# Kernel tuning notes

Hardware: AMD Instinct MI355X
Metric: run time of the kernel (lower is better)

Reference implementation:

```python
import jax, jax.numpy as jnp
import numpy as np

N_NODES = 100000
N_EDGES = 3200000
N_FEAT = 128
HIDDEN = 16
N_CLASSES = 10
N_GRAPHS = 64


def gcn_conv(x, W, b, src, dst, num_nodes):
    # PyG GCNConv: h = x W; add self-loops; norm = deg^{-1/2}[src]*deg^{-1/2}[dst]
    h = x @ W  # [N, out]
    deg = jax.ops.segment_sum(jnp.ones(src.shape[0], h.dtype), dst,
                              num_segments=num_nodes) + 1.0  # self-loop
    dinv = jax.lax.rsqrt(deg)
    coef = dinv[src] * dinv[dst]  # [E]
    agg = jax.ops.segment_sum(h[src] * coef[:, None], dst,
                              num_segments=num_nodes)
    # self-loop contribution: norm = dinv[i]^2
    agg = agg + h * (dinv * dinv)[:, None]
    return agg + b


def setup_inputs() -> dict:
    key = jax.random.key(0)
    k1, k2, k3, k4, k5, k6, k7 = jax.random.split(key, 7)
    x = jax.random.normal(k1, (N_NODES, N_FEAT), dtype=jnp.float32)
    edge_index = jax.random.randint(k2, (2, N_EDGES), 0, N_NODES, dtype=jnp.int64)
    batch = jnp.sort(jax.random.randint(k3, (N_NODES,), 0, N_GRAPHS, dtype=jnp.int64))
    W1 = jax.random.normal(k4, (N_FEAT, HIDDEN), dtype=jnp.float32) / np.sqrt(N_FEAT)
    b1 = jnp.zeros((HIDDEN,), jnp.float32)
    W2 = jax.random.normal(k5, (HIDDEN, N_CLASSES), dtype=jnp.float32) / np.sqrt(HIDDEN)
    b2 = jnp.zeros((N_CLASSES,), jnp.float32)
    return {"x": x, "edge_index": edge_index, "batch": batch,
            "W1": W1, "b1": b1, "W2": W2, "b2": b2}


def reference(x, edge_index, batch, W1, b1, W2, b2):
    src, dst = edge_index[0], edge_index[1]
    h = gcn_conv(x, W1, b1, src, dst, N_NODES)
    h = jax.nn.relu(h)
    h = gcn_conv(h, W2, b2, src, dst, N_NODES)  # [N, C]
    # global mean pool per graph
    sums = jax.ops.segment_sum(h, batch, num_segments=N_GRAPHS)
    cnts = jax.ops.segment_sum(jnp.ones(N_NODES, h.dtype), batch,
                               num_segments=N_GRAPHS)
    pooled = sums / jnp.maximum(cnts, 1.0)[:, None]  # [G, C]
    return jax.nn.log_softmax(pooled, axis=1)
```

## Files before the change

kernel.cpp:

```cpp
#include <hip/hip_runtime.h>

#define N_NODES   100000
#define N_EDGES   3200000
#define N_FEAT    128
#define HIDDEN    16
#define N_CLASSES 10
#define N_GRAPHS  64

#define NBUCK     391
#define CAP       9216
#define BINA_EPB  8192
#define BINA_BLOCKS ((N_EDGES + BINA_EPB - 1) / BINA_EPB)


__global__ __launch_bounds__(512) void k_ginit(int* __restrict__ gcur,
                                               float* __restrict__ pooled) {
    int t = threadIdx.x;
    if (t < NBUCK) gcur[t] = t * CAP;
    pooled[t] = 0.f;
    pooled[t + 512] = 0.f;
}

__global__ __launch_bounds__(512) void k_binA(const int* __restrict__ src,
                                              const int* __restrict__ dst,
                                              int* __restrict__ gcur,
                                              int* __restrict__ stage) {
    __shared__ int hist[NBUCK];
    __shared__ int curb[NBUCK];
    int tid = threadIdx.x;
    long long base = (long long)blockIdx.x * BINA_EPB;
    for (int t = tid; t < NBUCK; t += 512) hist[t] = 0;
    __syncthreads();
    int se[16], de[16];
#pragma unroll
    for (int i = 0; i < 16; ++i) {
        long long e = base + i * 512 + tid;
        if (e < N_EDGES) {
            se[i] = src[e];
            de[i] = dst[e];
            atomicAdd(&hist[de[i] >> 8], 1);
        } else {
            de[i] = -1;
        }
    }
    __syncthreads();
    for (int t = tid; t < NBUCK; t += 512) {
        int h = hist[t];
        curb[t] = h ? atomicAdd(&gcur[t], h) : 0;
    }
    __syncthreads();
#pragma unroll
    for (int i = 0; i < 16; ++i) {
        if (de[i] >= 0) {
            int b = de[i] >> 8;
            int p = atomicAdd(&curb[b], 1);
            stage[p] = (se[i] << 8) | (de[i] & 255);
        }
    }
}

__global__ __launch_bounds__(512) void k_bscan(const int* __restrict__ gcur,
                                               int* __restrict__ bbase,
                                               int* __restrict__ off) {
    __shared__ int s[512];
    int t = threadIdx.x;
    int c = (t < NBUCK) ? (gcur[t] - t * CAP) : 0;
    s[t] = c;
    __syncthreads();
    for (int o = 1; o < 512; o <<= 1) {
        int a = (t >= o) ? s[t - o] : 0;
        __syncthreads();
        s[t] += a;
        __syncthreads();
    }
    if (t < NBUCK) bbase[t] = s[t] - c;
    if (t == 0) off[N_NODES] = N_EDGES;
}

__global__ __launch_bounds__(256) void k_binB(const int* __restrict__ gcur,
                                              const int* __restrict__ bbase,
                                              const int* __restrict__ stage,
                                              int* __restrict__ off,
                                              float* __restrict__ dinv,
                                              int* __restrict__ srcs) {
    __shared__ int hist[256];
    __shared__ int excl[256];
    int b = blockIdx.x, t = threadIdx.x;
    int cnt   = gcur[b] - b * CAP;
    int sbase = b * CAP;
    int cbase = bbase[b];
    hist[t] = 0;
    __syncthreads();
    for (int i = t; i < cnt; i += 256) {
        int v = stage[sbase + i];
        atomicAdd(&hist[v & 255], 1);
    }
    __syncthreads();
    int c = hist[t];
    excl[t] = c;
    __syncthreads();
    for (int o = 1; o < 256; o <<= 1) {
        int a = (t >= o) ? excl[t - o] : 0;
        __syncthreads();
        excl[t] += a;
        __syncthreads();
    }
    int ex = excl[t] - c;
    int node = b * 256 + t;
    if (node < N_NODES) {
        off[node]  = cbase + ex;
        dinv[node] = rsqrtf((float)c + 1.0f);
    }
    __syncthreads();
    hist[t] = ex;
    __syncthreads();
    for (int i = t; i < cnt; i += 256) {
        int v = stage[sbase + i];
        int p = cbase + atomicAdd(&hist[v & 255], 1);
        srcs[p] = v >> 8;
    }
}

__global__ __launch_bounds__(256) void k_gemm1(const float* __restrict__ x,
                                               const float* __restrict__ W1,
                                               const float* __restrict__ dinv,
                                               float* __restrict__ h1p) {
    __shared__ float w[N_FEAT * HIDDEN];
    __shared__ float xs[16 * N_FEAT];
    __shared__ float ds[16];
    int tid  = threadIdx.x;
    int base = blockIdx.x * 16;
    if (tid < 16) ds[tid] = dinv[base + tid];
    const float4* w4 = (const float4*)W1;
    float4*       wd = (float4*)w;
    wd[tid]       = w4[tid];
    wd[256 + tid] = w4[256 + tid];
    const float4* x4 = (const float4*)(x + (long long)base * N_FEAT);
    float4*       xd = (float4*)xs;
    xd[tid]       = x4[tid];
    xd[256 + tid] = x4[256 + tid];
    __syncthreads();
    int n = tid >> 4, c = tid & 15;
    const float* xr = &xs[n * N_FEAT];
    float acc = 0.f;
#pragma unroll
    for (int k = 0; k < N_FEAT; ++k) acc += xr[k] * w[k * HIDDEN + c];
    h1p[(base + n) * HIDDEN + c] = acc * ds[n];
}

__global__ __launch_bounds__(256) void k_agg1(const int* __restrict__ off,
                                              const int* __restrict__ srcs,
                                              const float* __restrict__ dinv,
                                              const float* __restrict__ h1p,
                                              const float* __restrict__ b1,
                                              const float* __restrict__ W2,
                                              float* __restrict__ h2p) {
    __shared__ float r_s[16][17];
    __shared__ float w2s[HIDDEN * N_CLASSES];
    int tid = threadIdx.x;
    if (tid < HIDDEN * N_CLASSES) w2s[tid] = W2[tid];
    int nl = tid >> 4, c = tid & 15;
    int n  = blockIdx.x * 16 + nl;
    int beg = off[n], end = off[n + 1];
    float a0 = h1p[n * 16 + c];
    float a1 = 0.f, a2 = 0.f, a3 = 0.f;
    int j = beg;
    for (; j + 3 < end; j += 4) {
        int s0 = srcs[j], s1 = srcs[j + 1], s2 = srcs[j + 2], s3 = srcs[j + 3];
        a0 += h1p[s0 * 16 + c];
        a1 += h1p[s1 * 16 + c];
        a2 += h1p[s2 * 16 + c];
        a3 += h1p[s3 * 16 + c];
    }
    for (; j < end; ++j) a0 += h1p[srcs[j] * 16 + c];
    float acc = (a0 + a1) + (a2 + a3);
    float dn  = dinv[n];
    r_s[nl][c] = fmaxf(dn * acc + b1[c], 0.f);
    __syncthreads();
    if (c < N_CLASSES) {
        float o = 0.f;
#pragma unroll
        for (int k = 0; k < HIDDEN; ++k) o += r_s[nl][k] * w2s[k * N_CLASSES + c];
        h2p[n * 16 + c] = dn * o;
    } else {
        h2p[n * 16 + c] = 0.f;
    }
}

__global__ __launch_bounds__(256) void k_agg2p(const int* __restrict__ off,
                                               const int* __restrict__ srcs,
                                               const float* __restrict__ dinv,
                                               const float* __restrict__ h2p,
                                               const int* __restrict__ batch,
                                               float* __restrict__ pooled) {
    __shared__ float red[16][17];
    int tid = threadIdx.x;
    int nl = tid >> 4, c = tid & 15;
    int nbase = blockIdx.x * 16;
    int n  = nbase + nl;
    int beg = off[n], end = off[n + 1];
    float a0 = h2p[n * 16 + c];
    float a1 = 0.f, a2 = 0.f, a3 = 0.f;
    int j = beg;
    for (; j + 3 < end; j += 4) {
        int s0 = srcs[j], s1 = srcs[j + 1], s2 = srcs[j + 2], s3 = srcs[j + 3];
        a0 += h2p[s0 * 16 + c];
        a1 += h2p[s1 * 16 + c];
        a2 += h2p[s2 * 16 + c];
        a3 += h2p[s3 * 16 + c];
    }
    for (; j < end; ++j) a0 += h2p[srcs[j] * 16 + c];
    float o = dinv[n] * ((a0 + a1) + (a2 + a3));

    int g0  = batch[nbase];
    int g15 = batch[nbase + 15];
    if (g0 == g15) {
        red[nl][c] = o;
        __syncthreads();
#pragma unroll
        for (int s = 8; s > 0; s >>= 1) {
            if (nl < s) red[nl][c] += red[nl + s][c];
            __syncthreads();
        }
        if (tid < N_CLASSES) atomicAdd(&pooled[g0 * 16 + tid], red[0][tid]);
    } else {
        if (c < N_CLASSES) atomicAdd(&pooled[batch[n] * 16 + c], o);
    }
}

__global__ __launch_bounds__(64) void k_final(const float* __restrict__ pooled,
                                              const float* __restrict__ b2,
                                              const int* __restrict__ batch,
                                              float* __restrict__ out) {
    int g = threadIdx.x;
    if (g >= N_GRAPHS) return;
    int lo = 0, hi = N_NODES;
    while (lo < hi) { int m = (lo + hi) >> 1; if (batch[m] < g) lo = m + 1; else hi = m; }
    int start = lo;
    lo = 0; hi = N_NODES;
    while (lo < hi) { int m = (lo + hi) >> 1; if (batch[m] < g + 1) lo = m + 1; else hi = m; }
    int cnt = lo - start;

    float v[N_CLASSES];
    if (cnt > 0) {
        float inv = 1.f / (float)cnt;
#pragma unroll
        for (int j = 0; j < N_CLASSES; ++j) v[j] = pooled[g * 16 + j] * inv + b2[j];
    } else {
#pragma unroll
        for (int j = 0; j < N_CLASSES; ++j) v[j] = 0.f;
    }
    float m = v[0];
#pragma unroll
    for (int j = 1; j < N_CLASSES; ++j) m = fmaxf(m, v[j]);
    float l = 0.f;
#pragma unroll
    for (int j = 0; j < N_CLASSES; ++j) l += expf(v[j] - m);
    l = logf(l);
#pragma unroll
    for (int j = 0; j < N_CLASSES; ++j) out[g * N_CLASSES + j] = v[j] - m - l;
}

extern "C" void kernel_launch(void* const* d_in, const int* in_sizes, int n_in,
                              void* d_out, int out_size, void* d_ws, size_t ws_size,
                              hipStream_t stream) {
    const float* x     = (const float*)d_in[0];
    const int*   edge  = (const int*)d_in[1];
    const int*   batch = (const int*)d_in[2];
    const float* W1    = (const float*)d_in[3];
    const float* b1    = (const float*)d_in[4];
    const float* W2    = (const float*)d_in[5];
    const float* b2    = (const float*)d_in[6];
    float* out = (float*)d_out;
    float* ws  = (float*)d_ws;

    int*   gcur   = (int*)ws;
    int*   bbase  = (int*)(ws + 512);
    float* pooled = ws + 1024;
    float* dinv   = ws + 2048;
    int*   off    = (int*)(ws + 102048);
    int*   srcs   = (int*)(ws + 202080);
    int*   stage  = (int*)(ws + 3402080);
    float* h1p    = ws + 3402080;
    float* h2p    = ws + 5002080;

    const int* srcp = edge;
    const int* dstp = edge + N_EDGES;

    k_ginit<<<1, 512, 0, stream>>>(gcur, pooled);
    k_binA<<<BINA_BLOCKS, 512, 0, stream>>>(srcp, dstp, gcur, stage);
    k_bscan<<<1, 512, 0, stream>>>(gcur, bbase, off);
    k_binB<<<NBUCK, 256, 0, stream>>>(gcur, bbase, stage, off, dinv, srcs);
    k_gemm1<<<N_NODES / 16, 256, 0, stream>>>(x, W1, dinv, h1p);
    k_agg1<<<N_NODES / 16, 256, 0, stream>>>(off, srcs, dinv, h1p, b1, W2, h2p);
    k_agg2p<<<N_NODES / 16, 256, 0, stream>>>(off, srcs, dinv, h2p, batch, pooled);
    k_final<<<1, 64, 0, stream>>>(pooled, b2, batch, out);
}
```

Measured before the change: 282.1 us.

## Split feature tables into column halves to shrink gather working sets

The 16-wide hidden and class feature tables are split into separate column slices (8+8 for layer one, 8+2 for layer two). Each aggregation now runs as two passes, each gathering from a smaller table that is more likely to stay in cache, and the second layer no longer gathers padded zero columns. Edge index loads and intermediate stores are marked nontemporal. In exchange the CSR index array is read twice per layer, there are more kernel launches, and an extra intermediate buffer is written and read back.

```diff
diff --git a/kernel.cpp b/kernel.cpp
--- a/kernel.cpp
+++ b/kernel.cpp
@@ -124,7 +124,8 @@
 __global__ __launch_bounds__(256) void k_gemm1(const float* __restrict__ x,
                                                const float* __restrict__ W1,
                                                const float* __restrict__ dinv,
-                                               float* __restrict__ h1p) {
+                                               float* __restrict__ h1pA,
+                                               float* __restrict__ h1pB) {
     __shared__ float w[N_FEAT * HIDDEN];
     __shared__ float xs[16 * N_FEAT];
     __shared__ float ds[16];
@@ -145,86 +146,174 @@
     float acc = 0.f;
 #pragma unroll
     for (int k = 0; k < N_FEAT; ++k) acc += xr[k] * w[k * HIDDEN + c];
-    h1p[(base + n) * HIDDEN + c] = acc * ds[n];
-}
-
-__global__ __launch_bounds__(256) void k_agg1(const int* __restrict__ off,
-                                              const int* __restrict__ srcs,
-                                              const float* __restrict__ dinv,
-                                              const float* __restrict__ h1p,
-                                              const float* __restrict__ b1,
-                                              const float* __restrict__ W2,
-                                              float* __restrict__ h2p) {
-    __shared__ float r_s[16][17];
-    __shared__ float w2s[HIDDEN * N_CLASSES];
-    int tid = threadIdx.x;
-    if (tid < HIDDEN * N_CLASSES) w2s[tid] = W2[tid];
-    int nl = tid >> 4, c = tid & 15;
-    int n  = blockIdx.x * 16 + nl;
+    float v = acc * ds[n];
+    int nn = base + n;
+    if (c < 8) h1pA[nn * 8 + c] = v;
+    else       h1pB[nn * 8 + (c - 8)] = v;
+}
+
+__global__ __launch_bounds__(256) void k_agg1A(const int* __restrict__ off,
+                                               const int* __restrict__ srcs,
+                                               const float* __restrict__ h1pA,
+                                               float* __restrict__ aggA) {
+    int tid = threadIdx.x;
+    int nl = tid >> 3, c = tid & 7;
+    int n  = blockIdx.x * 32 + nl;
     int beg = off[n], end = off[n + 1];
-    float a0 = h1p[n * 16 + c];
+    float a0 = h1pA[n * 8 + c];
     float a1 = 0.f, a2 = 0.f, a3 = 0.f;
     int j = beg;
     for (; j + 3 < end; j += 4) {
-        int s0 = srcs[j], s1 = srcs[j + 1], s2 = srcs[j + 2], s3 = srcs[j + 3];
-        a0 += h1p[s0 * 16 + c];
-        a1 += h1p[s1 * 16 + c];
-        a2 += h1p[s2 * 16 + c];
-        a3 += h1p[s3 * 16 + c];
-    }
-    for (; j < end; ++j) a0 += h1p[srcs[j] * 16 + c];
-    float acc = (a0 + a1) + (a2 + a3);
-    float dn  = dinv[n];
-    r_s[nl][c] = fmaxf(dn * acc + b1[c], 0.f);
-    __syncthreads();
-    if (c < N_CLASSES) {
-        float o = 0.f;
-#pragma unroll
-        for (int k = 0; k < HIDDEN; ++k) o += r_s[nl][k] * w2s[k * N_CLASSES + c];
-        h2p[n * 16 + c] = dn * o;
-    } else {
-        h2p[n * 16 + c] = 0.f;
-    }
-}
-
-__global__ __launch_bounds__(256) void k_agg2p(const int* __restrict__ off,
+        int s0 = __builtin_nontemporal_load(&srcs[j]);
+        int s1 = __builtin_nontemporal_load(&srcs[j + 1]);
+        int s2 = __builtin_nontemporal_load(&srcs[j + 2]);
+        int s3 = __builtin_nontemporal_load(&srcs[j + 3]);
+        a0 += h1pA[s0 * 8 + c];
+        a1 += h1pA[s1 * 8 + c];
+        a2 += h1pA[s2 * 8 + c];
+        a3 += h1pA[s3 * 8 + c];
+    }
+    for (; j < end; ++j) a0 += h1pA[srcs[j] * 8 + c];
+    __builtin_nontemporal_store((a0 + a1) + (a2 + a3), &aggA[n * 8 + c]);
+}
+
+__global__ __launch_bounds__(256) void k_agg1B(const int* __restrict__ off,
                                                const int* __restrict__ srcs,
                                                const float* __restrict__ dinv,
-                                               const float* __restrict__ h2p,
-                                               const int* __restrict__ batch,
-                                               float* __restrict__ pooled) {
-    __shared__ float red[16][17];
-    int tid = threadIdx.x;
-    int nl = tid >> 4, c = tid & 15;
-    int nbase = blockIdx.x * 16;
-    int n  = nbase + nl;
+                                               const float* __restrict__ h1pB,
+                                               const float* __restrict__ aggA,
+                                               const float* __restrict__ b1,
+                                               const float* __restrict__ W2,
+                                               float* __restrict__ h2pA,
+                                               float* __restrict__ h2pB) {
+    __shared__ float r_s[32][17];
+    __shared__ float w2s[HIDDEN * N_CLASSES];
+    int tid = threadIdx.x;
+    if (tid < HIDDEN * N_CLASSES) w2s[tid] = W2[tid];
+    int nl = tid >> 3, c = tid & 7;
+    int n  = blockIdx.x * 32 + nl;
     int beg = off[n], end = off[n + 1];
-    float a0 = h2p[n * 16 + c];
+    float a0 = h1pB[n * 8 + c];
     float a1 = 0.f, a2 = 0.f, a3 = 0.f;
     int j = beg;
     for (; j + 3 < end; j += 4) {
-        int s0 = srcs[j], s1 = srcs[j + 1], s2 = srcs[j + 2], s3 = srcs[j + 3];
-        a0 += h2p[s0 * 16 + c];
-        a1 += h2p[s1 * 16 + c];
-        a2 += h2p[s2 * 16 + c];
-        a3 += h2p[s3 * 16 + c];
-    }
-    for (; j < end; ++j) a0 += h2p[srcs[j] * 16 + c];
+        int s0 = __builtin_nontemporal_load(&srcs[j]);
+        int s1 = __builtin_nontemporal_load(&srcs[j + 1]);
+        int s2 = __builtin_nontemporal_load(&srcs[j + 2]);
+        int s3 = __builtin_nontemporal_load(&srcs[j + 3]);
+        a0 += h1pB[s0 * 8 + c];
+        a1 += h1pB[s1 * 8 + c];
+        a2 += h1pB[s2 * 8 + c];
+        a3 += h1pB[s3 * 8 + c];
+    }
+    for (; j < end; ++j) a0 += h1pB[srcs[j] * 8 + c];
+    float sb = (a0 + a1) + (a2 + a3);
+    float sa = __builtin_nontemporal_load(&aggA[n * 8 + c]);
+    float dn = dinv[n];
+    r_s[nl][c]     = fmaxf(dn * sa + b1[c], 0.f);
+    r_s[nl][c + 8] = fmaxf(dn * sb + b1[c + 8], 0.f);
+    __syncthreads();
+    float o = 0.f;
+#pragma unroll
+    for (int k = 0; k < HIDDEN; ++k) o += r_s[nl][k] * w2s[k * N_CLASSES + c];
+    __builtin_nontemporal_store(dn * o, &h2pA[n * 8 + c]);
+    if (c < 2) {
+        float o2 = 0.f;
+#pragma unroll
+        for (int k = 0; k < HIDDEN; ++k) o2 += r_s[nl][k] * w2s[k * N_CLASSES + 8 + c];
+        __builtin_nontemporal_store(dn * o2, &h2pB[n * 2 + c]);
+    }
+}
+
+__global__ __launch_bounds__(256) void k_agg2A(const int* __restrict__ off,
+                                               const int* __restrict__ srcs,
+                                               const float* __restrict__ dinv,
+                                               const float* __restrict__ h2pA,
+                                               const int* __restrict__ batch,
+                                               float* __restrict__ pooled) {
+    __shared__ float red[32][9];
+    int tid = threadIdx.x;
+    int nl = tid >> 3, c = tid & 7;
+    int nbase = blockIdx.x * 32;
+    int n  = nbase + nl;
+    int beg = off[n], end = off[n + 1];
+    float a0 = h2pA[n * 8 + c];
+    float a1 = 0.f, a2 = 0.f, a3 = 0.f;
+    int j = beg;
+    for (; j + 3 < end; j += 4) {
+        int s0 = __builtin_nontemporal_load(&srcs[j]);
+        int s1 = __builtin_nontemporal_load(&srcs[j + 1]);
+        int s2 = __builtin_nontemporal_load(&srcs[j + 2]);
+        int s3 = __builtin_nontemporal_load(&srcs[j + 3]);
+        a0 += h2pA[s0 * 8 + c];
+        a1 += h2pA[s1 * 8 + c];
+        a2 += h2pA[s2 * 8 + c];
+        a3 += h2pA[s3 * 8 + c];
+    }
+    for (; j < end; ++j) a0 += h2pA[srcs[j] * 8 + c];
     float o = dinv[n] * ((a0 + a1) + (a2 + a3));
 
-    int g0  = batch[nbase];
-    int g15 = batch[nbase + 15];
-    if (g0 == g15) {
+    int g0 = batch[nbase];
+    int gL = batch[nbase + 31];
+    if (g0 == gL) {
         red[nl][c] = o;
         __syncthreads();
 #pragma unroll
-        for (int s = 8; s > 0; s >>= 1) {
+        for (int s = 16; s > 0; s >>= 1) {
             if (nl < s) red[nl][c] += red[nl + s][c];
             __syncthreads();
         }
-        if (tid < N_CLASSES) atomicAdd(&pooled[g0 * 16 + tid], red[0][tid]);
+        if (tid < 8) atomicAdd(&pooled[g0 * 16 + tid], red[0][tid]);
     } else {
-        if (c < N_CLASSES) atomicAdd(&pooled[batch[n] * 16 + c], o);
+        atomicAdd(&pooled[batch[n] * 16 + c], o);
+    }
+}
+
+__global__ __launch_bounds__(256) void k_agg2B(const int* __restrict__ off,
+                                               const int* __restrict__ srcs,
+                                               const float* __restrict__ dinv,
+                                               const float* __restrict__ h2pB,
+                                               const int* __restrict__ batch,
+                                               float* __restrict__ pooled) {
+    __shared__ float red[128][3];
+    int tid = threadIdx.x;
+    int nl = tid >> 1, c = tid & 1;
+    int nbase = blockIdx.x * 128;
+    int n  = nbase + nl;
+    float o = 0.f;
+    if (n < N_NODES) {
+        int beg = off[n], end = off[n + 1];
+        float a0 = h2pB[n * 2 + c];
+        float a1 = 0.f, a2 = 0.f, a3 = 0.f;
+        int j = beg;
+        for (; j + 3 < end; j += 4) {
+            int s0 = __builtin_nontemporal_load(&srcs[j]);
+            int s1 = __builtin_nontemporal_load(&srcs[j + 1]);
+            int s2 = __builtin_nontemporal_load(&srcs[j + 2]);
+            int s3 = __builtin_nontemporal_load(&srcs[j + 3]);
+            a0 += h2pB[s0 * 2 + c];
+            a1 += h2pB[s1 * 2 + c];
+            a2 += h2pB[s2 * 2 + c];
+            a3 += h2pB[s3 * 2 + c];
+        }
+        for (; j < end; ++j) a0 += h2pB[srcs[j] * 2 + c];
+        o = dinv[n] * ((a0 + a1) + (a2 + a3));
+    }
+    int nLast = nbase + 127;
+    if (nLast >= N_NODES) nLast = N_NODES - 1;
+    int g0 = batch[nbase];
+    int gL = batch[nLast];
+    if (g0 == gL) {
+        red[nl][c] = o;
+        __syncthreads();
+#pragma unroll
+        for (int s = 64; s > 0; s >>= 1) {
+            if (nl < s) red[nl][c] += red[nl + s][c];
+            __syncthreads();
+        }
+        if (tid < 2) atomicAdd(&pooled[g0 * 16 + 8 + tid], red[0][tid]);
+    } else {
+        if (n < N_NODES) atomicAdd(&pooled[batch[n] * 16 + 8 + c], o);
     }
 }
 
@@ -281,8 +370,11 @@
     int*   off    = (int*)(ws + 102048);
     int*   srcs   = (int*)(ws + 202080);
     int*   stage  = (int*)(ws + 3402080);
-    float* h1p    = ws + 3402080;
-    float* h2p    = ws + 5002080;
+    float* h1pA   = ws + 3402080;
+    float* h1pB   = ws + 4202080;
+    float* aggA   = ws + 5002080;
+    float* h2pA   = ws + 5802080;
+    float* h2pB   = ws + 6602080;
 
     const int* srcp = edge;
     const int* dstp = edge + N_EDGES;
@@ -291,8 +383,10 @@
     k_binA<<<BINA_BLOCKS, 512, 0, stream>>>(srcp, dstp, gcur, stage);
     k_bscan<<<1, 512, 0, stream>>>(gcur, bbase, off);
     k_binB<<<NBUCK, 256, 0, stream>>>(gcur, bbase, stage, off, dinv, srcs);
-    k_gemm1<<<N_NODES / 16, 256, 0, stream>>>(x, W1, dinv, h1p);
-    k_agg1<<<N_NODES / 16, 256, 0, stream>>>(off, srcs, dinv, h1p, b1, W2, h2p);
-    k_agg2p<<<N_NODES / 16, 256, 0, stream>>>(off, srcs, dinv, h2p, batch, pooled);
+    k_gemm1<<<N_NODES / 16, 256, 0, stream>>>(x, W1, dinv, h1pA, h1pB);
+    k_agg1A<<<N_NODES / 32, 256, 0, stream>>>(off, srcs, h1pA, aggA);
+    k_agg1B<<<N_NODES / 32, 256, 0, stream>>>(off, srcs, dinv, h1pB, aggA, b1, W2, h2pA, h2pB);
+    k_agg2A<<<N_NODES / 32, 256, 0, stream>>>(off, srcs, dinv, h2pA, batch, pooled);
+    k_agg2B<<<(N_NODES + 127) / 128, 256, 0, stream>>>(off, srcs, dinv, h2pB, batch, pooled);
     k_final<<<1, 64, 0, stream>>>(pooled, b2, batch, out);
 }
```

Result: slower. 370.1 us (+31.2%).

## Store hidden features in fp16 and gather with vectorized edge-parallel lanes

Applied to the files above, without the earlier changes.

Intermediate node features h1/h2 are stored as half precision, halving the bytes moved by the random gathers in both aggregation kernels. Each node's 16 lanes now split edges eight ways, with each lane loading 8 halves as one 16-byte vector, using nontemporal index loads, and the partial sums are combined with xor shuffles. The binning kernel also doubles edges per block and threads per block. The risks are precision loss from fp16 storage and extra synchronisation and shuffle overhead per node.

```diff
diff --git a/kernel.cpp b/kernel.cpp
--- a/kernel.cpp
+++ b/kernel.cpp
@@ -1,4 +1,5 @@
 #include <hip/hip_runtime.h>
+#include <hip/hip_fp16.h>
 
 #define N_NODES   100000
 #define N_EDGES   3200000
@@ -9,7 +10,7 @@
 
 #define NBUCK     391
 #define CAP       9216
-#define BINA_EPB  8192
+#define BINA_EPB  16384
 #define BINA_BLOCKS ((N_EDGES + BINA_EPB - 1) / BINA_EPB)
 
 
@@ -21,20 +22,20 @@
     pooled[t + 512] = 0.f;
 }
 
-__global__ __launch_bounds__(512) void k_binA(const int* __restrict__ src,
-                                              const int* __restrict__ dst,
-                                              int* __restrict__ gcur,
-                                              int* __restrict__ stage) {
+__global__ __launch_bounds__(1024) void k_binA(const int* __restrict__ src,
+                                               const int* __restrict__ dst,
+                                               int* __restrict__ gcur,
+                                               int* __restrict__ stage) {
     __shared__ int hist[NBUCK];
     __shared__ int curb[NBUCK];
     int tid = threadIdx.x;
     long long base = (long long)blockIdx.x * BINA_EPB;
-    for (int t = tid; t < NBUCK; t += 512) hist[t] = 0;
+    for (int t = tid; t < NBUCK; t += 1024) hist[t] = 0;
     __syncthreads();
     int se[16], de[16];
 #pragma unroll
     for (int i = 0; i < 16; ++i) {
-        long long e = base + i * 512 + tid;
+        long long e = base + i * 1024 + tid;
         if (e < N_EDGES) {
             se[i] = src[e];
             de[i] = dst[e];
@@ -44,7 +45,7 @@
         }
     }
     __syncthreads();
-    for (int t = tid; t < NBUCK; t += 512) {
+    for (int t = tid; t < NBUCK; t += 1024) {
         int h = hist[t];
         curb[t] = h ? atomicAdd(&gcur[t], h) : 0;
     }
@@ -124,7 +125,7 @@
 __global__ __launch_bounds__(256) void k_gemm1(const float* __restrict__ x,
                                                const float* __restrict__ W1,
                                                const float* __restrict__ dinv,
-                                               float* __restrict__ h1p) {
+                                               __half* __restrict__ h1h) {
     __shared__ float w[N_FEAT * HIDDEN];
     __shared__ float xs[16 * N_FEAT];
     __shared__ float ds[16];
@@ -145,86 +146,116 @@
     float acc = 0.f;
 #pragma unroll
     for (int k = 0; k < N_FEAT; ++k) acc += xr[k] * w[k * HIDDEN + c];
-    h1p[(base + n) * HIDDEN + c] = acc * ds[n];
-}
+    h1h[(base + n) * HIDDEN + c] = __float2half(acc * ds[n]);
+}
+
+#define NT(p) __builtin_nontemporal_load(p)
+
+#define GATHER_DEF(TBL)                                                       \
+    float acc[8];                                                             \
+    _Pragma("unroll") for (int q = 0; q < 8; ++q) acc[q] = 0.f;               \
+    {                                                                         \
+        int ne = end - beg;                                                   \
+        int nr = ne >> 3;                                                     \
+        int j  = beg + k;                                                     \
+        int npair = nr >> 1;                                                  \
+        if (npair > 0) {                                                      \
+            int sA = NT(&srcs[j]), sB = NT(&srcs[j + 8]);                     \
+            for (int p = 1; p < npair; ++p) {                                 \
+                int sC = NT(&srcs[j + 16]), sD = NT(&srcs[j + 24]);           \
+                GACC(TBL, sA); GACC(TBL, sB);                                 \
+                sA = sC; sB = sD; j += 16;                                    \
+            }                                                                 \
+            GACC(TBL, sA); GACC(TBL, sB); j += 16;                            \
+        }                                                                     \
+        if (nr & 1) { int sA = NT(&srcs[j]); GACC(TBL, sA); j += 8; }         \
+        if (k < (ne & 7)) { int sA = NT(&srcs[j]); GACC(TBL, sA); }           \
+    }                                                                         \
+    _Pragma("unroll") for (int m = 2; m <= 8; m <<= 1) {                      \
+        _Pragma("unroll") for (int q = 0; q < 8; ++q)                         \
+            acc[q] += __shfl_xor(acc[q], m, 64);                              \
+    }
+
+#define GACC(TBL, S) {                                                        \
+    float4 g_ = *(const float4*)(&TBL[(S) * 16 + h * 8]);                     \
+    const __half2* hp_ = (const __half2*)&g_;                                 \
+    float2 v0_ = __half22float2(hp_[0]);                                      \
+    float2 v1_ = __half22float2(hp_[1]);                                      \
+    float2 v2_ = __half22float2(hp_[2]);                                      \
+    float2 v3_ = __half22float2(hp_[3]);                                      \
+    acc[0] += v0_.x; acc[1] += v0_.y; acc[2] += v1_.x; acc[3] += v1_.y;       \
+    acc[4] += v2_.x; acc[5] += v2_.y; acc[6] += v3_.x; acc[7] += v3_.y; }
 
 __global__ __launch_bounds__(256) void k_agg1(const int* __restrict__ off,
                                               const int* __restrict__ srcs,
                                               const float* __restrict__ dinv,
-                                              const float* __restrict__ h1p,
+                                              const __half* __restrict__ h1h,
                                               const float* __restrict__ b1,
                                               const float* __restrict__ W2,
-                                              float* __restrict__ h2p) {
+                                              __half* __restrict__ h2h) {
     __shared__ float r_s[16][17];
     __shared__ float w2s[HIDDEN * N_CLASSES];
     int tid = threadIdx.x;
     if (tid < HIDDEN * N_CLASSES) w2s[tid] = W2[tid];
-    int nl = tid >> 4, c = tid & 15;
+    int nl = tid >> 4, l = tid & 15, k = l >> 1, h = l & 1;
     int n  = blockIdx.x * 16 + nl;
     int beg = off[n], end = off[n + 1];
-    float a0 = h1p[n * 16 + c];
-    float a1 = 0.f, a2 = 0.f, a3 = 0.f;
-    int j = beg;
-    for (; j + 3 < end; j += 4) {
-        int s0 = srcs[j], s1 = srcs[j + 1], s2 = srcs[j + 2], s3 = srcs[j + 3];
-        a0 += h1p[s0 * 16 + c];
-        a1 += h1p[s1 * 16 + c];
-        a2 += h1p[s2 * 16 + c];
-        a3 += h1p[s3 * 16 + c];
-    }
-    for (; j < end; ++j) a0 += h1p[srcs[j] * 16 + c];
-    float acc = (a0 + a1) + (a2 + a3);
-    float dn  = dinv[n];
-    r_s[nl][c] = fmaxf(dn * acc + b1[c], 0.f);
-    __syncthreads();
-    if (c < N_CLASSES) {
-        float o = 0.f;
-#pragma unroll
-        for (int k = 0; k < HIDDEN; ++k) o += r_s[nl][k] * w2s[k * N_CLASSES + c];
-        h2p[n * 16 + c] = dn * o;
-    } else {
-        h2p[n * 16 + c] = 0.f;
-    }
+    GATHER_DEF(h1h)
+    if (l < 2) {
+#pragma unroll
+        for (int q = 0; q < 8; ++q) r_s[nl][h * 8 + q] = acc[q];
+    }
+    __syncthreads();
+    float dn   = dinv[n];
+    float self = __half2float(h1h[n * 16 + l]);
+    float val  = fmaxf(dn * (r_s[nl][l] + self) + b1[l], 0.f);
+    __syncthreads();
+    r_s[nl][l] = val;
+    __syncthreads();
+    float o = 0.f;
+    if (l < N_CLASSES) {
+#pragma unroll
+        for (int q = 0; q < HIDDEN; ++q) o += r_s[nl][q] * w2s[q * N_CLASSES + l];
+        o *= dn;
+    }
+    h2h[n * 16 + l] = __float2half(o);
 }
 
 __global__ __launch_bounds__(256) void k_agg2p(const int* __restrict__ off,
                                                const int* __restrict__ srcs,
                                                const float* __restrict__ dinv,
-                                               const float* __restrict__ h2p,
+                                               const __half* __restrict__ h2h,
                                                const int* __restrict__ batch,
                                                float* __restrict__ pooled) {
     __shared__ float red[16][17];
     int tid = threadIdx.x;
-    int nl = tid >> 4, c = tid & 15;
+    int nl = tid >> 4, l = tid & 15, k = l >> 1, h = l & 1;
     int nbase = blockIdx.x * 16;
     int n  = nbase + nl;
     int beg = off[n], end = off[n + 1];
-    float a0 = h2p[n * 16 + c];
-    float a1 = 0.f, a2 = 0.f, a3 = 0.f;
-    int j = beg;
-    for (; j + 3 < end; j += 4) {
-        int s0 = srcs[j], s1 = srcs[j + 1], s2 = srcs[j + 2], s3 = srcs[j + 3];
-        a0 += h2p[s0 * 16 + c];
-        a1 += h2p[s1 * 16 + c];
-        a2 += h2p[s2 * 16 + c];
-        a3 += h2p[s3 * 16 + c];
-    }
-    for (; j < end; ++j) a0 += h2p[srcs[j] * 16 + c];
-    float o = dinv[n] * ((a0 + a1) + (a2 + a3));
+    GATHER_DEF(h2h)
+    if (l < 2) {
+#pragma unroll
+        for (int q = 0; q < 8; ++q) red[nl][h * 8 + q] = acc[q];
+    }
+    __syncthreads();
+    float self = __half2float(h2h[n * 16 + l]);
+    float o = dinv[n] * (red[nl][l] + self);
+    __syncthreads();
 
     int g0  = batch[nbase];
     int g15 = batch[nbase + 15];
     if (g0 == g15) {
-        red[nl][c] = o;
+        red[nl][l] = o;
         __syncthreads();
 #pragma unroll
         for (int s = 8; s > 0; s >>= 1) {
-            if (nl < s) red[nl][c] += red[nl + s][c];
+            if (nl < s) red[nl][l] += red[nl + s][l];
             __syncthreads();
         }
         if (tid < N_CLASSES) atomicAdd(&pooled[g0 * 16 + tid], red[0][tid]);
     } else {
-        if (c < N_CLASSES) atomicAdd(&pooled[batch[n] * 16 + c], o);
+        if (l < N_CLASSES) atomicAdd(&pooled[batch[n] * 16 + l], o);
     }
 }
 
@@ -274,25 +305,25 @@
     float* out = (float*)d_out;
     float* ws  = (float*)d_ws;
 
-    int*   gcur   = (int*)ws;
-    int*   bbase  = (int*)(ws + 512);
-    float* pooled = ws + 1024;
-    float* dinv   = ws + 2048;
-    int*   off    = (int*)(ws + 102048);
-    int*   srcs   = (int*)(ws + 202080);
-    int*   stage  = (int*)(ws + 3402080);
-    float* h1p    = ws + 3402080;
-    float* h2p    = ws + 5002080;
+    int*    gcur   = (int*)ws;
+    int*    bbase  = (int*)(ws + 512);
+    float*  pooled = ws + 1024;
+    float*  dinv   = ws + 2048;
+    int*    off    = (int*)(ws + 102048);
+    int*    srcs   = (int*)(ws + 202080);
+    int*    stage  = (int*)(ws + 3402080);
+    __half* h1h    = (__half*)(ws + 3402080);
+    __half* h2h    = (__half*)(ws + 4202080);
 
     const int* srcp = edge;
     const int* dstp = edge + N_EDGES;
 
     k_ginit<<<1, 512, 0, stream>>>(gcur, pooled);
-    k_binA<<<BINA_BLOCKS, 512, 0, stream>>>(srcp, dstp, gcur, stage);
+    k_binA<<<BINA_BLOCKS, 1024, 0, stream>>>(srcp, dstp, gcur, stage);
     k_bscan<<<1, 512, 0, stream>>>(gcur, bbase, off);
     k_binB<<<NBUCK, 256, 0, stream>>>(gcur, bbase, stage, off, dinv, srcs);
-    k_gemm1<<<N_NODES / 16, 256, 0, stream>>>(x, W1, dinv, h1p);
-    k_agg1<<<N_NODES / 16, 256, 0, stream>>>(off, srcs, dinv, h1p, b1, W2, h2p);
-    k_agg2p<<<N_NODES / 16, 256, 0, stream>>>(off, srcs, dinv, h2p, batch, pooled);
+    k_gemm1<<<N_NODES / 16, 256, 0, stream>>>(x, W1, dinv, h1h);
+    k_agg1<<<N_NODES / 16, 256, 0, stream>>>(off, srcs, dinv, h1h, b1, W2, h2h);
+    k_agg2p<<<N_NODES / 16, 256, 0, stream>>>(off, srcs, dinv, h2h, batch, pooled);
     k_final<<<1, 64, 0, stream>>>(pooled, b2, batch, out);
 }
```

New measurement: 249.1 us. -11.7%, faster.
